# Optimization experiments

Measured on AMD Instinct MI355X. Metric: run time of the kernel, lower is better.

## Reference

```python
import jax, jax.numpy as jnp
import numpy as np
from jax import lax


def _upsample2x(x):
    # PyTorch nn.Upsample(scale_factor=2, mode='bilinear', align_corners=False) on NCHW
    B, C, H, W = x.shape
    def idx_w(n):
        src = (jnp.arange(2 * n, dtype=jnp.float32) + 0.5) / 2.0 - 0.5
        src = jnp.clip(src, 0.0, n - 1)
        i0 = jnp.floor(src).astype(jnp.int32)
        i1 = jnp.minimum(i0 + 1, n - 1)
        t = src - i0.astype(jnp.float32)
        return i0, i1, t
    r0, r1, ty = idx_w(H)
    c0, c1, tx = idx_w(W)
    xr = x[:, :, r0, :] * (1.0 - ty)[None, None, :, None] + x[:, :, r1, :] * ty[None, None, :, None]
    return xr[:, :, :, c0] * (1.0 - tx) + xr[:, :, :, c1] * tx


def _disco_conv_s2(x, psi_idx, psi_val, w, b, hw):
    # DISCO spherical conv: irregular neighbor gather + quadrature-weighted basis
    # contraction, then small GEMM over (in_channels, kernel basis).
    B, C, H, W = x.shape
    xf = x.reshape(B, C, H * W)
    g = xf[:, :, psi_idx]                      # [B,C,P,N] irregular gather
    z = jnp.einsum('bcpn,kpn->bckp', g, psi_val)  # [B,C,K,P]
    y = jnp.einsum('bckp,ock->bop', z, w) + b[None, :, None]
    return y.reshape(B, w.shape[0], hw[0], hw[1])


def _conv2d_same(x, w, b):
    y = lax.conv_general_dilated(x, w, (1, 1), 'SAME',
                                 dimension_numbers=('NCHW', 'OIHW', 'NCHW'))
    return y + b[None, :, None, None]


def _srcnn(x, psi_idx, psi_val, wd, bd, cw2, cb2, cw3, cb3, hw):
    x = jax.nn.relu(_disco_conv_s2(x, psi_idx, psi_val, wd, bd, hw))
    x = jax.nn.relu(_conv2d_same(x, cw2, cb2))
    return _conv2d_same(x, cw3, cb3)


def setup_inputs() -> dict:
    key = jax.random.key(0)
    ks = jax.random.split(key, 16)
    H0, W0 = 90, 180
    P1 = (2 * H0) * (2 * W0)          # 64800
    P2 = (4 * H0) * (4 * W0)          # 259200
    K, NNZ, F = 9, 8, 64
    inp = {
        'x': jax.random.normal(ks[0], (4, 1, H0, W0), jnp.float32),
        'elev0': jax.random.normal(ks[1], (4, 1, 2 * H0, 2 * W0), jnp.float32),
        'elev1': jax.random.normal(ks[2], (4, 1, 4 * H0, 4 * W0), jnp.float32),
        'psi_idx1': jax.random.randint(ks[3], (P1, NNZ), 0, P1, jnp.int32),
        'psi_val1': jax.random.uniform(ks[4], (K, P1, NNZ), jnp.float32) * 0.1,
        'w1': jax.random.normal(ks[5], (F, 2, K), jnp.float32) * 0.1,
        'b1': jnp.zeros((F,), jnp.float32),
        'cw2_1': jax.random.normal(ks[6], (F // 2, F, 5, 5), jnp.float32) * 0.02,
        'cb2_1': jnp.zeros((F // 2,), jnp.float32),
        'cw3_1': jax.random.normal(ks[7], (1, F // 2, 5, 5), jnp.float32) * 0.02,
        'cb3_1': jnp.zeros((1,), jnp.float32),
        'psi_idx2': jax.random.randint(ks[8], (P2, NNZ), 0, P2, jnp.int32),
        'psi_val2': jax.random.uniform(ks[9], (K, P2, NNZ), jnp.float32) * 0.1,
        'w2': jax.random.normal(ks[10], (F, 2, K), jnp.float32) * 0.1,
        'b2': jnp.zeros((F,), jnp.float32),
        'cw2_2': jax.random.normal(ks[11], (F // 2, F, 5, 5), jnp.float32) * 0.02,
        'cb2_2': jnp.zeros((F // 2,), jnp.float32),
        'cw3_2': jax.random.normal(ks[12], (1, F // 2, 5, 5), jnp.float32) * 0.02,
        'cb3_2': jnp.zeros((1,), jnp.float32),
    }
    return inp


def reference(x, elev0, elev1, psi_idx1, psi_val1, w1, b1, cw2_1, cb2_1, cw3_1, cb3_1,
              psi_idx2, psi_val2, w2, b2, cw2_2, cb2_2, cw3_2, cb3_2):
    h = _upsample2x(x)
    h = jnp.concatenate([h, elev0], axis=1)
    h = _srcnn(h, psi_idx1, psi_val1, w1, b1, cw2_1, cb2_1, cw3_1, cb3_1, (180, 360))
    # Stage 2
    h = _upsample2x(h)
    h = jnp.concatenate([h, elev1], axis=1)
    h = _srcnn(h, psi_idx2, psi_val2, w2, b2, cw2_2, cb2_2, cw3_2, cb3_2, (360, 720))
    return h
```

## Files before the change

### kernel.cpp

```cpp
#include <hip/hip_runtime.h>
#include <hip/hip_bf16.h>

typedef __hip_bfloat16 bf16;
typedef __attribute__((ext_vector_type(8))) short short8;
typedef __attribute__((ext_vector_type(4))) short short4v;
typedef __attribute__((ext_vector_type(4))) float float4v;

__device__ __forceinline__ short f2bs(float x) {
    bf16 b = __float2bfloat16(x);
    return *reinterpret_cast<short*>(&b);
}

__device__ __forceinline__ void wave_lds_fence() {
    __builtin_amdgcn_wave_barrier();
    __builtin_amdgcn_s_waitcnt(0xC07F);
    __builtin_amdgcn_wave_barrier();
}

__global__ void upsample_pack_k(const float* __restrict__ in,
                                const float* __restrict__ elev,
                                float* __restrict__ out2, int B, int H, int W) {
    const int OH = 2 * H, OW = 2 * W;
    const long total = (long)B * OH * OW;
    long i = (long)blockIdx.x * blockDim.x + threadIdx.x;
    if (i >= total) return;
    int ox = (int)(i % OW);
    long r = i / OW;
    int oy = (int)(r % OH);
    int b  = (int)(r / OH);
    float sy = fminf(fmaxf(oy * 0.5f - 0.25f, 0.0f), (float)(H - 1));
    float sx = fminf(fmaxf(ox * 0.5f - 0.25f, 0.0f), (float)(W - 1));
    int y0 = (int)sy; float ty = sy - (float)y0; int y1 = min(y0 + 1, H - 1);
    int x0 = (int)sx; float tx = sx - (float)x0; int x1 = min(x0 + 1, W - 1);
    const float* p = in + (size_t)b * H * W;
    float v00 = p[(size_t)y0 * W + x0];
    float v01 = p[(size_t)y0 * W + x1];
    float v10 = p[(size_t)y1 * W + x0];
    float v11 = p[(size_t)y1 * W + x1];
    float v = (v00 * (1.f - ty) + v10 * ty) * (1.f - tx)
            + (v01 * (1.f - ty) + v11 * ty) * tx;
    float2 o; o.x = v; o.y = elev[i];
    *(float2*)(out2 + i * 2) = o;
}

__global__ void packall_k(const float* __restrict__ cw2_1, const float* __restrict__ cw2_2,
                          const float* __restrict__ cw3_1, const float* __restrict__ cw3_2,
                          const float* __restrict__ w1,    const float* __restrict__ w2,
                          short* __restrict__ wfA,  short* __restrict__ wfB,
                          short* __restrict__ wf31, short* __restrict__ wf32,
                          short* __restrict__ wfD1, short* __restrict__ wfD2) {
    int gi = blockIdx.x * 256 + threadIdx.x;
    if (gi < 102400) {
        const float* src = (gi < 51200) ? cw2_1 : cw2_2;
        short* dst       = (gi < 51200) ? wfA   : wfB;
        int i = (gi < 51200) ? gi : gi - 51200;
        int j    = i & 7;
        int r    = i >> 3;
        int lane = r & 63;
        int r2   = r >> 6;
        int mt   = r2 & 1;
        int r3   = r2 >> 1;
        int tap  = r3 % 25;
        int icc  = r3 / 25;
        int m = lane & 15, q = lane >> 4;
        int oc = mt * 16 + m;
        int ic = icc * 32 + q * 8 + j;
        dst[i] = f2bs(src[((size_t)oc * 64 + ic) * 25 + tap]);
    } else if (gi < 128000) {
        int gi2 = gi - 102400;
        const float* src = (gi2 < 12800) ? cw3_1 : cw3_2;
        short* dst       = (gi2 < 12800) ? wf31  : wf32;
        int i = (gi2 < 12800) ? gi2 : gi2 - 12800;
        int j    = i & 7;
        int r    = i >> 3;
        int lane = r & 63;
        int tap  = r >> 6;
        int m = lane & 15, q = lane >> 4;
        dst[i] = (m == 0) ? f2bs(src[(size_t)(q * 8 + j) * 25 + tap]) : (short)0;
    } else if (gi < 132096) {
        int gi2 = gi - 128000;
        const float* src = (gi2 < 2048) ? w1 : w2;
        short* dst       = (gi2 < 2048) ? wfD1 : wfD2;
        int i = (gi2 < 2048) ? gi2 : gi2 - 2048;
        int j = i & 7;
        int r = i >> 3;
        int lane = r & 63;
        int mtile = r >> 6;
        int q = lane >> 4, mm = lane & 15;
        int oc = mtile * 16 + mm;
        int k = q * 8 + j;
        dst[i] = (k < 18) ? f2bs(src[oc * 18 + k]) : (short)0;
    }
}

__global__ __launch_bounds__(256)
void disco_k(const float* __restrict__ ui,
             const int* __restrict__ psi_idx, const float* __restrict__ psi_val,
             const short* __restrict__ wfragD, const float* __restrict__ bias,
             short* __restrict__ outh, int P) {
    __shared__ short zs[256 * 40];
    const int tid  = threadIdx.x;
    const int lane = tid & 63;
    const int wv   = tid >> 6;
    const int q    = lane >> 4;
    const int n    = lane & 15;

    for (int c0 = 0; c0 < 40; c0 += 8) *(short8*)(zs + tid * 40 + c0) = (short8)0;

    short8 af[4];
    float brg[4][4];
    #pragma unroll
    for (int mt = 0; mt < 4; mt++) {
        af[mt] = *(const short8*)(wfragD + ((mt * 64 + lane) << 3));
        #pragma unroll
        for (int r = 0; r < 4; r++) brg[mt][r] = bias[mt * 16 + q * 4 + r];
    }

    const int p = blockIdx.x * 256 + tid;
    const bool valid = p < P;

    int idx[8];
    float pv[9][8];
    if (valid) {
        const int* ip = psi_idx + (size_t)p * 8;
        int4 ia = *(const int4*)ip;
        int4 ib = *(const int4*)(ip + 4);
        idx[0]=ia.x; idx[1]=ia.y; idx[2]=ia.z; idx[3]=ia.w;
        idx[4]=ib.x; idx[5]=ib.y; idx[6]=ib.z; idx[7]=ib.w;
        #pragma unroll
        for (int k = 0; k < 9; k++) {
            const float* qp = psi_val + ((size_t)k * P + p) * 8;
            float4 qa = *(const float4*)qp;
            float4 qb = *(const float4*)(qp + 4);
            pv[k][0]=qa.x; pv[k][1]=qa.y; pv[k][2]=qa.z; pv[k][3]=qa.w;
            pv[k][4]=qb.x; pv[k][5]=qb.y; pv[k][6]=qb.z; pv[k][7]=qb.w;
        }
    }

    for (int bq = 0; bq < 4; bq++) {
        if (valid) {
            const float* ub = ui + (size_t)bq * P * 2;
            float g0[8], g1[8];
            #pragma unroll
            for (int t = 0; t < 8; t++) {
                float2 g = *(const float2*)(ub + (size_t)idx[t] * 2);
                g0[t] = g.x; g1[t] = g.y;
            }
            float z[18];
            #pragma unroll
            for (int j = 0; j < 18; j++) z[j] = 0.f;
            #pragma unroll
            for (int k = 0; k < 9; k++) {
                #pragma unroll
                for (int t = 0; t < 8; t++) {
                    z[k]     = fmaf(g0[t], pv[k][t], z[k]);
                    z[9 + k] = fmaf(g1[t], pv[k][t], z[9 + k]);
                }
            }
            #pragma unroll
            for (int c0i = 0; c0i < 16; c0i += 4) {
                short4v t4;
                t4.x = f2bs(z[c0i]); t4.y = f2bs(z[c0i+1]);
                t4.z = f2bs(z[c0i+2]); t4.w = f2bs(z[c0i+3]);
                *(short4v*)(zs + tid * 40 + c0i) = t4;
            }
            unsigned int lo = (unsigned short)f2bs(z[16]);
            unsigned int hi = (unsigned short)f2bs(z[17]);
            *(unsigned int*)(zs + tid * 40 + 16) = lo | (hi << 16);
        }
        wave_lds_fence();

        #pragma unroll
        for (int t = 0; t < 4; t++) {
            const int nt  = wv * 4 + t;
            const int pix = blockIdx.x * 256 + nt * 16 + n;
            short8 bz = *(const short8*)(zs + (nt * 16 + n) * 40 + q * 8);
            const bool pok = pix < P;
            short* hp = outh + ((size_t)bq * P + pix) * 64;
            #pragma unroll
            for (int mt = 0; mt < 4; mt++) {
                float4v acc = {0.f, 0.f, 0.f, 0.f};
                acc = __builtin_amdgcn_mfma_f32_16x16x32_bf16(af[mt], bz, acc, 0, 0, 0);
                if (pok) {
                    short4v o;
                    o.x = f2bs(fmaxf(acc.x + brg[mt][0], 0.f));
                    o.y = f2bs(fmaxf(acc.y + brg[mt][1], 0.f));
                    o.z = f2bs(fmaxf(acc.z + brg[mt][2], 0.f));
                    o.w = f2bs(fmaxf(acc.w + brg[mt][3], 0.f));
                    *(short4v*)(hp + mt * 16 + q * 4) = o;
                }
            }
        }
        wave_lds_fence();
    }
}

__global__ __launch_bounds__(256, 4)
void conv2_k(const short* __restrict__ hS, const short* __restrict__ wfrag,
             const float* __restrict__ bias, short* __restrict__ outc,
             int H, int W) {
    __shared__ short slab[12 * 36 * 40];
    const int tid  = threadIdx.x;
    const int wv   = tid >> 6;
    const int lane = tid & 63;
    const int q    = lane >> 4;
    const int n    = lane & 15;
    const int xbase = blockIdx.x * 32;
    const int ybase = blockIdx.y * 8;
    const int b     = blockIdx.z;
    const short* hb = hS + (size_t)b * H * W * 64;

    float4v acc[2][2][2];
    #pragma unroll
    for (int ri = 0; ri < 2; ri++)
        #pragma unroll
        for (int nt = 0; nt < 2; nt++)
            #pragma unroll
            for (int mt = 0; mt < 2; mt++)
                acc[ri][nt][mt] = (float4v){0.f, 0.f, 0.f, 0.f};

    float brg[2][4];
    #pragma unroll
    for (int mt = 0; mt < 2; mt++)
        #pragma unroll
        for (int r = 0; r < 4; r++) brg[mt][r] = bias[mt * 16 + q * 4 + r];

    for (int icc = 0; icc < 2; icc++) {
        __syncthreads();
        for (int l = tid; l < 1728; l += 256) {
            int qq  = l & 3;
            int pix = l >> 2;
            int row = pix / 36;
            int col = pix - row * 36;
            int gy = ybase - 2 + row;
            int gx = xbase - 2 + col;
            short8 v = (short8)0;
            if ((unsigned)gy < (unsigned)H && (unsigned)gx < (unsigned)W)
                v = *(const short8*)(hb + ((size_t)gy * W + gx) * 64 + icc * 32 + qq * 8);
            *(short8*)(slab + pix * 40 + qq * 8) = v;
        }
        __syncthreads();

        const short* wfr = wfrag + (size_t)icc * 25600;
        #pragma unroll
        for (int t = 0; t < 6; t++) {
            const int srow = wv * 2 + t;
            #pragma unroll
            for (int kx = 0; kx < 5; kx++) {
                short8 w0a, w0b, w1a, w1b;
                if (t <= 4) {
                    const int tp = t * 5 + kx;
                    w0a = *(const short8*)(wfr + ((tp * 2 + 0) * 64 + lane) * 8);
                    w0b = *(const short8*)(wfr + ((tp * 2 + 1) * 64 + lane) * 8);
                }
                if (t >= 1) {
                    const int tp = (t - 1) * 5 + kx;
                    w1a = *(const short8*)(wfr + ((tp * 2 + 0) * 64 + lane) * 8);
                    w1b = *(const short8*)(wfr + ((tp * 2 + 1) * 64 + lane) * 8);
                }
                const int boff = (srow * 36 + n + kx) * 40 + q * 8;
                #pragma unroll
                for (int nt = 0; nt < 2; nt++) {
                    short8 bfr = *(const short8*)(slab + boff + nt * 640);
                    if (t <= 4) {
                        acc[0][nt][0] = __builtin_amdgcn_mfma_f32_16x16x32_bf16(w0a, bfr, acc[0][nt][0], 0, 0, 0);
                        acc[0][nt][1] = __builtin_amdgcn_mfma_f32_16x16x32_bf16(w0b, bfr, acc[0][nt][1], 0, 0, 0);
                    }
                    if (t >= 1) {
                        acc[1][nt][0] = __builtin_amdgcn_mfma_f32_16x16x32_bf16(w1a, bfr, acc[1][nt][0], 0, 0, 0);
                        acc[1][nt][1] = __builtin_amdgcn_mfma_f32_16x16x32_bf16(w1b, bfr, acc[1][nt][1], 0, 0, 0);
                    }
                }
            }
        }
    }

    #pragma unroll
    for (int ri = 0; ri < 2; ri++) {
        const int y = ybase + wv * 2 + ri;
        if (y < H) {
            #pragma unroll
            for (int nt = 0; nt < 2; nt++) {
                const int x = xbase + nt * 16 + n;
                if (x < W) {
                    short* cp = outc + (((size_t)b * H * W + (size_t)y * W + x) * 32);
                    #pragma unroll
                    for (int mt = 0; mt < 2; mt++) {
                        short4v o;
                        o.x = f2bs(fmaxf(acc[ri][nt][mt].x + brg[mt][0], 0.f));
                        o.y = f2bs(fmaxf(acc[ri][nt][mt].y + brg[mt][1], 0.f));
                        o.z = f2bs(fmaxf(acc[ri][nt][mt].z + brg[mt][2], 0.f));
                        o.w = f2bs(fmaxf(acc[ri][nt][mt].w + brg[mt][3], 0.f));
                        *(short4v*)(cp + mt * 16 + q * 4) = o;
                    }
                }
            }
        }
    }
}

__global__ __launch_bounds__(256, 4)
void conv3_k(const short* __restrict__ cP, const short* __restrict__ wf3,
             const float* __restrict__ bias, float* __restrict__ out,
             int H, int W) {
    __shared__ short slab[12 * 36 * 40];
    const int tid  = threadIdx.x;
    const int wv   = tid >> 6;
    const int lane = tid & 63;
    const int q    = lane >> 4;
    const int n    = lane & 15;
    const int xbase = blockIdx.x * 32;
    const int ybase = blockIdx.y * 8;
    const int b     = blockIdx.z;
    const short* cb = cP + (size_t)b * H * W * 32;

    for (int l = tid; l < 1728; l += 256) {
        int qq  = l & 3;
        int pix = l >> 2;
        int row = pix / 36;
        int col = pix - row * 36;
        int gy = ybase - 2 + row;
        int gx = xbase - 2 + col;
        short8 v = (short8)0;
        if ((unsigned)gy < (unsigned)H && (unsigned)gx < (unsigned)W)
            v = *(const short8*)(cb + ((size_t)gy * W + gx) * 32 + qq * 8);
        *(short8*)(slab + pix * 40 + qq * 8) = v;
    }
    __syncthreads();

    float4v acc[2][2];
    #pragma unroll
    for (int ri = 0; ri < 2; ri++)
        #pragma unroll
        for (int nt = 0; nt < 2; nt++) acc[ri][nt] = (float4v){0.f, 0.f, 0.f, 0.f};

    #pragma unroll
    for (int t = 0; t < 6; t++) {
        const int srow = wv * 2 + t;
        #pragma unroll
        for (int kx = 0; kx < 5; kx++) {
            short8 a0, a1;
            if (t <= 4) a0 = *(const short8*)(wf3 + (((t * 5 + kx) * 64 + lane)) * 8);
            if (t >= 1) a1 = *(const short8*)(wf3 + ((((t - 1) * 5 + kx) * 64 + lane)) * 8);
            const int boff = (srow * 36 + n + kx) * 40 + q * 8;
            #pragma unroll
            for (int nt = 0; nt < 2; nt++) {
                short8 bfr = *(const short8*)(slab + boff + nt * 640);
                if (t <= 4) acc[0][nt] = __builtin_amdgcn_mfma_f32_16x16x32_bf16(a0, bfr, acc[0][nt], 0, 0, 0);
                if (t >= 1) acc[1][nt] = __builtin_amdgcn_mfma_f32_16x16x32_bf16(a1, bfr, acc[1][nt], 0, 0, 0);
            }
        }
    }

    const float bi = bias[0];
    if (q == 0) {
        #pragma unroll
        for (int ri = 0; ri < 2; ri++) {
            const int y = ybase + wv * 2 + ri;
            if (y < H) {
                #pragma unroll
                for (int nt = 0; nt < 2; nt++) {
                    const int x = xbase + nt * 16 + n;
                    if (x < W) out[((size_t)b * H + y) * W + x] = acc[ri][nt].x + bi;
                }
            }
        }
    }
}

extern "C" void kernel_launch(void* const* d_in, const int* in_sizes, int n_in,
                              void* d_out, int out_size, void* d_ws, size_t ws_size,
                              hipStream_t stream) {
    const float* x        = (const float*)d_in[0];
    const float* elev0    = (const float*)d_in[1];
    const float* elev1    = (const float*)d_in[2];
    const int*   psi_idx1 = (const int*)  d_in[3];
    const float* psi_val1 = (const float*)d_in[4];
    const float* w1       = (const float*)d_in[5];
    const float* b1       = (const float*)d_in[6];
    const float* cw2_1    = (const float*)d_in[7];
    const float* cb2_1    = (const float*)d_in[8];
    const float* cw3_1    = (const float*)d_in[9];
    const float* cb3_1    = (const float*)d_in[10];
    const int*   psi_idx2 = (const int*)  d_in[11];
    const float* psi_val2 = (const float*)d_in[12];
    const float* w2       = (const float*)d_in[13];
    const float* b2       = (const float*)d_in[14];
    const float* cw2_2    = (const float*)d_in[15];
    const float* cb2_2    = (const float*)d_in[16];
    const float* cw3_2    = (const float*)d_in[17];
    const float* cb3_2    = (const float*)d_in[18];

    const int B = 4;
    const int H1 = 180, W1 = 360, P1 = H1 * W1;
    const int H2 = 360, W2 = 720, P2 = H2 * W2;

    char* ws = (char*)d_ws;
    short* h    = (short*)(ws);
    short* c    = (short*)(ws + 132710400);
    float* u2i  = (float*)(ws + 149299200);
    float* u1i  = (float*)(ws + 199065600);
    float* s1   = (float*)(ws + 201139200);
    short* wfA  = (short*)(ws + 202176000);
    short* wfB  = (short*)(ws + 202278400);
    short* wfD1 = (short*)(ws + 202380800);
    short* wfD2 = (short*)(ws + 202384896);
    short* wf31 = (short*)(ws + 202388992);
    short* wf32 = (short*)(ws + 202414592);
    (void)ws_size; (void)in_sizes; (void)n_in; (void)out_size;

    packall_k<<<(132096 + 255) / 256, 256, 0, stream>>>(
        cw2_1, cw2_2, cw3_1, cw3_2, w1, w2, wfA, wfB, wf31, wf32, wfD1, wfD2);

    upsample_pack_k<<<(B * P1 + 255) / 256, 256, 0, stream>>>(x, elev0, u1i, B, 90, 180);
    disco_k<<<(P1 + 255) / 256, 256, 0, stream>>>(
        u1i, psi_idx1, psi_val1, wfD1, b1, h, P1);
    conv2_k<<<dim3((W1 + 31) / 32, (H1 + 7) / 8, B), 256, 0, stream>>>(
        h, wfA, cb2_1, c, H1, W1);
    conv3_k<<<dim3((W1 + 31) / 32, (H1 + 7) / 8, B), 256, 0, stream>>>(
        c, wf31, cb3_1, s1, H1, W1);

    upsample_pack_k<<<(B * P2 + 255) / 256, 256, 0, stream>>>(s1, elev1, u2i, B, H1, W1);
    disco_k<<<(P2 + 255) / 256, 256, 0, stream>>>(
        u2i, psi_idx2, psi_val2, wfD2, b2, h, P2);
    conv2_k<<<dim3((W2 + 31) / 32, (H2 + 7) / 8, B), 256, 0, stream>>>(
        h, wfB, cb2_2, c, H2, W2);
    conv3_k<<<dim3((W2 + 31) / 32, (H2 + 7) / 8, B), 256, 0, stream>>>(
        c, wf32, cb3_2, (float*)d_out, H2, W2);
}
```

Measured before the change: 491.9 us.

## Reorder conv loops by kx and double-buffer weight fragments in registers

Conv2 and conv3 now iterate over kx outermost and keep register buffers holding the weight fragments for every ky of the current kx. The next kx's weights are prefetched while the current kx's MFMAs run, and conv2 issues its first weight loads before the slab fill. The goal is to hide global weight-load latency behind MFMA work. The larger register footprint is why conv2's launch bounds drop from 4 to 3 blocks per SM, which cuts occupancy.

```diff
diff --git a/kernel.cpp b/kernel.cpp
--- a/kernel.cpp
+++ b/kernel.cpp
@@ -195,7 +195,7 @@
     }
 }
 
-__global__ __launch_bounds__(256, 4)
+__global__ __launch_bounds__(256, 3)
 void conv2_k(const short* __restrict__ hS, const short* __restrict__ wfrag,
              const float* __restrict__ bias, short* __restrict__ outc,
              int H, int W) {
@@ -226,6 +226,13 @@
         for (int r = 0; r < 4; r++) brg[mt][r] = bias[mt * 16 + q * 4 + r];
 
     for (int icc = 0; icc < 2; icc++) {
+        const short* wfr = wfrag + (size_t)icc * 25600;
+        short8 wbuf[2][5][2];
+        #pragma unroll
+        for (int ky = 0; ky < 5; ky++) {
+            wbuf[0][ky][0] = *(const short8*)(wfr + (((ky * 5) * 2 + 0) * 64 + lane) * 8);
+            wbuf[0][ky][1] = *(const short8*)(wfr + (((ky * 5) * 2 + 1) * 64 + lane) * 8);
+        }
         __syncthreads();
         for (int l = tid; l < 1728; l += 256) {
             int qq  = l & 3;
@@ -241,35 +248,32 @@
         }
         __syncthreads();
 
-        const short* wfr = wfrag + (size_t)icc * 25600;
-        #pragma unroll
-        for (int t = 0; t < 6; t++) {
-            const int srow = wv * 2 + t;
-            #pragma unroll
-            for (int kx = 0; kx < 5; kx++) {
-                short8 w0a, w0b, w1a, w1b;
+        #pragma unroll
+        for (int kx = 0; kx < 5; kx++) {
+            const int cur = kx & 1;
+            if (kx < 4) {
+                #pragma unroll
+                for (int ky = 0; ky < 5; ky++) {
+                    wbuf[cur ^ 1][ky][0] = *(const short8*)(wfr + (((ky * 5 + kx + 1) * 2 + 0) * 64 + lane) * 8);
+                    wbuf[cur ^ 1][ky][1] = *(const short8*)(wfr + (((ky * 5 + kx + 1) * 2 + 1) * 64 + lane) * 8);
+                }
+            }
+            #pragma unroll
+            for (int t = 0; t < 6; t++) {
+                const int boff = ((wv * 2 + t) * 36 + n + kx) * 40 + q * 8;
+                short8 b0 = *(const short8*)(slab + boff);
+                short8 b1 = *(const short8*)(slab + boff + 640);
                 if (t <= 4) {
-                    const int tp = t * 5 + kx;
-                    w0a = *(const short8*)(wfr + ((tp * 2 + 0) * 64 + lane) * 8);
-                    w0b = *(const short8*)(wfr + ((tp * 2 + 1) * 64 + lane) * 8);
+                    acc[0][0][0] = __builtin_amdgcn_mfma_f32_16x16x32_bf16(wbuf[cur][t][0], b0, acc[0][0][0], 0, 0, 0);
+                    acc[0][0][1] = __builtin_amdgcn_mfma_f32_16x16x32_bf16(wbuf[cur][t][1], b0, acc[0][0][1], 0, 0, 0);
+                    acc[0][1][0] = __builtin_amdgcn_mfma_f32_16x16x32_bf16(wbuf[cur][t][0], b1, acc[0][1][0], 0, 0, 0);
+                    acc[0][1][1] = __builtin_amdgcn_mfma_f32_16x16x32_bf16(wbuf[cur][t][1], b1, acc[0][1][1], 0, 0, 0);
                 }
                 if (t >= 1) {
-                    const int tp = (t - 1) * 5 + kx;
-                    w1a = *(const short8*)(wfr + ((tp * 2 + 0) * 64 + lane) * 8);
-                    w1b = *(const short8*)(wfr + ((tp * 2 + 1) * 64 + lane) * 8);
-                }
-                const int boff = (srow * 36 + n + kx) * 40 + q * 8;
-                #pragma unroll
-                for (int nt = 0; nt < 2; nt++) {
-                    short8 bfr = *(const short8*)(slab + boff + nt * 640);
-                    if (t <= 4) {
-                        acc[0][nt][0] = __builtin_amdgcn_mfma_f32_16x16x32_bf16(w0a, bfr, acc[0][nt][0], 0, 0, 0);
-                        acc[0][nt][1] = __builtin_amdgcn_mfma_f32_16x16x32_bf16(w0b, bfr, acc[0][nt][1], 0, 0, 0);
-                    }
-                    if (t >= 1) {
-                        acc[1][nt][0] = __builtin_amdgcn_mfma_f32_16x16x32_bf16(w1a, bfr, acc[1][nt][0], 0, 0, 0);
-                        acc[1][nt][1] = __builtin_amdgcn_mfma_f32_16x16x32_bf16(w1b, bfr, acc[1][nt][1], 0, 0, 0);
-                    }
+                    acc[1][0][0] = __builtin_amdgcn_mfma_f32_16x16x32_bf16(wbuf[cur][t - 1][0], b0, acc[1][0][0], 0, 0, 0);
+                    acc[1][0][1] = __builtin_amdgcn_mfma_f32_16x16x32_bf16(wbuf[cur][t - 1][1], b0, acc[1][0][1], 0, 0, 0);
+                    acc[1][1][0] = __builtin_amdgcn_mfma_f32_16x16x32_bf16(wbuf[cur][t - 1][0], b1, acc[1][1][0], 0, 0, 0);
+                    acc[1][1][1] = __builtin_amdgcn_mfma_f32_16x16x32_bf16(wbuf[cur][t - 1][1], b1, acc[1][1][1], 0, 0, 0);
                 }
             }
         }
@@ -314,6 +318,11 @@
     const int b     = blockIdx.z;
     const short* cb = cP + (size_t)b * H * W * 32;
 
+    short8 wbuf[2][5];
+    #pragma unroll
+    for (int ky = 0; ky < 5; ky++)
+        wbuf[0][ky] = *(const short8*)(wf3 + (((ky * 5) * 64 + lane)) * 8);
+
     for (int l = tid; l < 1728; l += 256) {
         int qq  = l & 3;
         int pix = l >> 2;
@@ -335,19 +344,25 @@
         for (int nt = 0; nt < 2; nt++) acc[ri][nt] = (float4v){0.f, 0.f, 0.f, 0.f};
 
     #pragma unroll
-    for (int t = 0; t < 6; t++) {
-        const int srow = wv * 2 + t;
-        #pragma unroll
-        for (int kx = 0; kx < 5; kx++) {
-            short8 a0, a1;
-            if (t <= 4) a0 = *(const short8*)(wf3 + (((t * 5 + kx) * 64 + lane)) * 8);
-            if (t >= 1) a1 = *(const short8*)(wf3 + ((((t - 1) * 5 + kx) * 64 + lane)) * 8);
-            const int boff = (srow * 36 + n + kx) * 40 + q * 8;
-            #pragma unroll
-            for (int nt = 0; nt < 2; nt++) {
-                short8 bfr = *(const short8*)(slab + boff + nt * 640);
-                if (t <= 4) acc[0][nt] = __builtin_amdgcn_mfma_f32_16x16x32_bf16(a0, bfr, acc[0][nt], 0, 0, 0);
-                if (t >= 1) acc[1][nt] = __builtin_amdgcn_mfma_f32_16x16x32_bf16(a1, bfr, acc[1][nt], 0, 0, 0);
+    for (int kx = 0; kx < 5; kx++) {
+        const int cur = kx & 1;
+        if (kx < 4) {
+            #pragma unroll
+            for (int ky = 0; ky < 5; ky++)
+                wbuf[cur ^ 1][ky] = *(const short8*)(wf3 + (((ky * 5 + kx + 1) * 64 + lane)) * 8);
+        }
+        #pragma unroll
+        for (int t = 0; t < 6; t++) {
+            const int boff = ((wv * 2 + t) * 36 + n + kx) * 40 + q * 8;
+            short8 b0 = *(const short8*)(slab + boff);
+            short8 b1 = *(const short8*)(slab + boff + 640);
+            if (t <= 4) {
+                acc[0][0] = __builtin_amdgcn_mfma_f32_16x16x32_bf16(wbuf[cur][t], b0, acc[0][0], 0, 0, 0);
+                acc[0][1] = __builtin_amdgcn_mfma_f32_16x16x32_bf16(wbuf[cur][t], b1, acc[0][1], 0, 0, 0);
+            }
+            if (t >= 1) {
+                acc[1][0] = __builtin_amdgcn_mfma_f32_16x16x32_bf16(wbuf[cur][t - 1], b0, acc[1][0], 0, 0, 0);
+                acc[1][1] = __builtin_amdgcn_mfma_f32_16x16x32_bf16(wbuf[cur][t - 1], b1, acc[1][1], 0, 0, 0);
             }
         }
     }
```

Measured after the change: 476.3 us. -3.2%, faster.
